# Kernel optimization log

Measured on AMD Instinct MI355X. Metric: run time of the kernel, lower is better.

Reference implementation:

```python
import jax, jax.numpy as jnp
import numpy as np

EMBED_DIM = 512
SMOOTH = 4.0        # args.lambda_softmax
LAMBDA_LSE = 6.0    # args.lambda_lse
LEAKY_SLOPE = 0.1
EPS = 1e-8


def setup_inputs() -> dict:
    key = jax.random.key(0)
    k1, k2, k3 = jax.random.split(key, 3)
    n_contract, n_region = 32, 256
    n_law, max_len = 32, 256
    contracts = jax.random.normal(k1, (n_contract, n_region, EMBED_DIM), jnp.float32)
    laws = jax.random.normal(k2, (n_law, max_len, EMBED_DIM), jnp.float32)
    law_lens = jax.random.randint(k3, (n_law,), 128, max_len + 1, jnp.int32)
    return {"contracts": contracts, "laws": laws, "law_lens": law_lens}


def reference(contracts, laws, law_lens):
    # contracts: [C, R, D], laws: [N, L, D], law_lens: [N]
    n_law, max_len, d = laws.shape
    # mask[n, l] = 1 if word l is within law n's true length
    mask = (jnp.arange(max_len)[None, :] < law_lens[:, None]).astype(contracts.dtype)

    # attn = law @ contract^T / sqrt(D): [N, C, L, R]
    attn = jnp.einsum('nld,crd->nclr', laws, contracts) / jnp.sqrt(jnp.float32(d))
    attn = jax.nn.leaky_relu(attn, LEAKY_SLOPE)
    # l2norm over region dim (per law-word row)
    attn = attn / (jnp.linalg.norm(attn, axis=-1, keepdims=True) + EPS)
    attn = jax.nn.softmax(attn, axis=-1) * SMOOTH
    # zero out contributions from padded law words (ragged lengths)
    attn = attn * mask[:, None, :, None]

    # weighted_law: [N, C, R, D]
    wlaw = jnp.einsum('nld,nclr->ncrd', laws, attn)

    # cosine similarity along D: [N, C, R]
    w12 = jnp.sum(contracts[None] * wlaw, axis=-1)
    w1 = jnp.linalg.norm(contracts, axis=-1)[None]          # [1, C, R]
    w2 = jnp.linalg.norm(wlaw, axis=-1)                      # [N, C, R]
    sim = w12 / jnp.maximum(w1 * w2, EPS)

    # LogSumExp aggregation over regions -> [N, C]
    row_sim = jnp.log(jnp.sum(jnp.exp(sim * LAMBDA_LSE), axis=-1)) / LAMBDA_LSE
    # concatenate per-law columns -> [C, N]
    return row_sim.T
```

## Files before the change

### kernel.cpp

```cpp
#include <hip/hip_runtime.h>
#include <hip/hip_bf16.h>

#define CN 32
#define RN 256
#define DN 512
#define NN 32
#define LN 256

#define STAGE_OFF 131072
#define SMEM_TOTAL 163840

typedef short v8s __attribute__((ext_vector_type(8)));
typedef float v4f __attribute__((ext_vector_type(4)));
typedef const __attribute__((address_space(1))) void* gas1_t;
typedef __attribute__((address_space(3))) void* las3_t;

__device__ __forceinline__ void gl2lds16(const void* g, void* l) {
  __builtin_amdgcn_global_load_lds((gas1_t)g, (las3_t)l, 16, 0, 0);
}

__device__ __forceinline__ unsigned short f2bf(float x) {
  unsigned int u = __float_as_uint(x);
  u = (u + 0x7fffu + ((u >> 16) & 1u)) >> 16;
  return (unsigned short)u;
}
__device__ __forceinline__ float bf2f(unsigned short h) {
  return __uint_as_float(((unsigned int)h) << 16);
}

__device__ __forceinline__ unsigned int pkbf(float a, float b) {
  __hip_bfloat162 h = __float22bfloat162_rn(make_float2(a, b));
  unsigned int u;
  __builtin_memcpy(&u, &h, sizeof(u));
  return u;
}

__device__ __forceinline__ const v8s* stgFrag(const unsigned short* buf, int r,
                                              int quad) {
  return (const v8s*)(buf + r * 32 + ((quad ^ ((r >> 1) & 3)) << 3));
}

__device__ __forceinline__ int satIdx(int r, int col) {
  return (r << 8) | ((((col >> 3) ^ (r & 7)) << 3) | (col & 7));
}

__device__ __forceinline__ v8s ldFrag64(const float* buf, int r, int cp) {
  const float* p = buf + r * 64 + (((cp + r) & 7) << 3);
  const float4 x0 = ((const float4*)p)[0];
  const float4 x1 = ((const float4*)p)[1];
  unsigned short h[8];
  h[0] = f2bf(x0.x); h[1] = f2bf(x0.y); h[2] = f2bf(x0.z); h[3] = f2bf(x0.w);
  h[4] = f2bf(x1.x); h[5] = f2bf(x1.y); h[6] = f2bf(x1.z); h[7] = f2bf(x1.w);
  return *(v8s*)h;
}

__global__ __launch_bounds__(512) void setup_kernel(
    const float* __restrict__ con, const float* __restrict__ laws,
    unsigned short* __restrict__ lawsB, unsigned short* __restrict__ conB,
    float* __restrict__ cnorm, unsigned short* __restrict__ G) {
  const int bid = blockIdx.x;
  const int t = threadIdx.x;
  if (bid < 256) {
    __shared__ float slice[256 * 64];
    const int n = bid >> 3;
    const int m0 = (bid & 7) << 5;
    const int lane = t & 63;
    const int w = t >> 6;
    const int quad = lane >> 4;
    const int l16 = lane & 15;
    const int rg = w >> 2;
    const int cg = w & 3;
    const float* lawN = laws + n * (LN * DN);

    v4f acc[4];
#pragma unroll
    for (int b = 0; b < 4; ++b) acc[b] = (v4f){0.f, 0.f, 0.f, 0.f};

    for (int ch = 0; ch < 8; ++ch) {
      const int dk = ch << 6;
      __syncthreads();
#pragma unroll
      for (int i = 0; i < 8; ++i) {
        const int s = i * 512 + t;
        const int row = s >> 4;
        const int p = s & 15;
        const int srcCol = ((((p >> 1) - row) & 7) << 3) + ((p & 1) << 2);
        gl2lds16(lawN + row * DN + dk + srcCol, (char*)slice + s * 16);
      }
      __syncthreads();
#pragma unroll
      for (int step = 0; step < 2; ++step) {
        const int cp = quad + (step << 2);
        v8s af = ldFrag64(slice, m0 + rg * 16 + l16, cp);
#pragma unroll
        for (int ct = 0; ct < 4; ++ct) {
          v8s bf = ldFrag64(slice, cg * 64 + ct * 16 + l16, cp);
          acc[ct] = __builtin_amdgcn_mfma_f32_16x16x32_bf16(af, bf, acc[ct], 0, 0, 0);
        }
      }
    }
    unsigned short* g = G + n * (LN * LN);
#pragma unroll
    for (int ct = 0; ct < 4; ++ct)
#pragma unroll
      for (int reg = 0; reg < 4; ++reg) {
        const int l = m0 + rg * 16 + quad * 4 + reg;
        g[l * LN + cg * 64 + ct * 16 + l16] = f2bf(acc[ct][reg]);
      }
  } else if (bid < 1280) {
    const int r = (bid - 256) * 8 + (t >> 6);
    const int lane = t & 63;
    const float4* src = (const float4*)(con + r * DN + lane * 8);
    float4 x0 = src[0], x1 = src[1];
    unsigned short h[8];
    h[0] = f2bf(x0.x); h[1] = f2bf(x0.y); h[2] = f2bf(x0.z); h[3] = f2bf(x0.w);
    h[4] = f2bf(x1.x); h[5] = f2bf(x1.y); h[6] = f2bf(x1.z); h[7] = f2bf(x1.w);
    *(v8s*)(conB + r * DN + lane * 8) = *(v8s*)h;
    float s = x0.x * x0.x + x0.y * x0.y + x0.z * x0.z + x0.w * x0.w +
              x1.x * x1.x + x1.y * x1.y + x1.z * x1.z + x1.w * x1.w;
#pragma unroll
    for (int m = 1; m < 64; m <<= 1) s += __shfl_xor(s, m, 64);
    if (lane == 0) cnorm[r] = sqrtf(s);
  } else {
    const int off = (bid - 1280) * 4096 + t * 8;
    const float4* src = (const float4*)(laws + off);
    float4 x0 = src[0], x1 = src[1];
    unsigned short h[8];
    h[0] = f2bf(x0.x); h[1] = f2bf(x0.y); h[2] = f2bf(x0.z); h[3] = f2bf(x0.w);
    h[4] = f2bf(x1.x); h[5] = f2bf(x1.y); h[6] = f2bf(x1.z); h[7] = f2bf(x1.w);
    *(v8s*)(lawsB + off) = *(v8s*)h;
  }
}

__global__ __launch_bounds__(512, 2) void main_kernel(
    const int* __restrict__ law_lens, const unsigned short* __restrict__ lawsB,
    const unsigned short* __restrict__ conB, const unsigned short* __restrict__ Gm,
    const float* __restrict__ cnorm, float* __restrict__ out) {
  extern __shared__ char smem[];
  unsigned short* sAt = (unsigned short*)smem;
  char* stage = smem + STAGE_OFF;

  const int bid = blockIdx.x;
  const int n = bid >> 5;
  const int c = bid & 31;
  const int t = threadIdx.x;
  const int lane = t & 63;
  const int w = t >> 6;
  const int quad = lane >> 4;
  const int l16 = lane & 15;
  const int sub = t & 3;
  const int rQ = t >> 2;
  const int subx = sub ^ ((rQ >> 1) & 3);
  const int len = law_lens[n];
  const int nCh = (len + 31) >> 5;
  const bool active = (w * 32) < len;

  const unsigned short* lawN = lawsB + n * (LN * DN);
  const unsigned short* conC = conB + c * (RN * DN);
  const unsigned short* Gn = Gm + n * (LN * LN);

  float w12p[16];
#pragma unroll
  for (int i = 0; i < 16; ++i) w12p[i] = 0.f;

  {
    const unsigned short* a0p = lawN + (w * 32 + l16) * DN + quad * 8;
    const unsigned short* a1p = a0p + 16 * DN;

    v4f acc[2][16];
#pragma unroll
    for (int a = 0; a < 2; ++a)
#pragma unroll
      for (int b = 0; b < 16; ++b) acc[a][b] = (v4f){0.f, 0.f, 0.f, 0.f};

#pragma unroll
    for (int i = 0; i < 2; ++i)
      gl2lds16(conC + (i * 128 + rQ) * DN + subx * 8,
               stage + i * 8192 + t * 16);

    for (int ch = 0; ch < 16; ++ch) {
      const int dk = ch << 5;
      __syncthreads();
      v8s af0 = *(const v8s*)(a0p + dk);
      v8s af1 = *(const v8s*)(a1p + dk);
      __builtin_amdgcn_sched_barrier(0);
      if (ch < 15) {
        char* dst = stage + ((ch + 1) & 1) * 16384;
#pragma unroll
        for (int i = 0; i < 2; ++i)
          gl2lds16(conC + (i * 128 + rQ) * DN + (dk + 32) + subx * 8,
                   dst + i * 8192 + t * 16);
      }
      __builtin_amdgcn_sched_barrier(0);
      if (active) {
        const unsigned short* cs =
            (const unsigned short*)(stage + (ch & 1) * 16384);
#pragma unroll
        for (int rt = 0; rt < 16; ++rt) {
          v8s bf = *stgFrag(cs, rt * 16 + l16, quad);
          acc[0][rt] = __builtin_amdgcn_mfma_f32_16x16x32_bf16(af0, bf, acc[0][rt], 0, 0, 0);
          acc[1][rt] = __builtin_amdgcn_mfma_f32_16x16x32_bf16(af1, bf, acc[1][rt], 0, 0, 0);
        }
      }
    }

    __syncthreads();

#pragma unroll
    for (int i = 0; i < 2; ++i)
      gl2lds16(Gn + (i * 128 + rQ) * LN + subx * 8, stage + i * 8192 + t * 16);

    if (active) {
#pragma unroll
      for (int tl = 0; tl < 2; ++tl) {
        unsigned int pk[16][2];
        float a0s[16];
#pragma unroll
        for (int reg = 0; reg < 4; ++reg) {
          const int lg = w * 32 + tl * 16 + quad * 4 + reg;
          float ss = 0.f;
#pragma unroll
          for (int rt = 0; rt < 16; ++rt) {
            const float v = acc[tl][rt][reg] * 0.04419417382415922f;
            const float lv = v > 0.f ? v : 0.1f * v;
            ss += lv * lv;
          }
#pragma unroll
          for (int m = 1; m < 16; m <<= 1) ss += __shfl_xor(ss, m, 64);
          const float inv = 1.f / (sqrtf(ss) + 1e-8f);
          float e[16];
          float den = 0.f;
#pragma unroll
          for (int rt = 0; rt < 16; ++rt) {
            const float v = acc[tl][rt][reg] * 0.04419417382415922f;
            const float lv = v > 0.f ? v : 0.1f * v;
            e[rt] = __expf(lv * inv);
            den += e[rt];
          }
#pragma unroll
          for (int m = 1; m < 16; m <<= 1) den += __shfl_xor(den, m, 64);
          const float sc = (lg < len) ? 4.f / den : 0.f;
#pragma unroll
          for (int rt = 0; rt < 16; ++rt) {
            const float v = acc[tl][rt][reg] * 0.04419417382415922f;
            const float a = e[rt] * sc;
            w12p[rt] += a * v;
            if (reg & 1)
              pk[rt][reg >> 1] = pkbf(a0s[rt], a);
            else
              a0s[rt] = a;
          }
        }
        const int lg0 = w * 32 + tl * 16 + quad * 4;
#pragma unroll
        for (int rt = 0; rt < 16; ++rt)
          *(uint2*)(sAt + satIdx(rt * 16 + l16, lg0)) = *(uint2*)pk[rt];
      }
    } else {
      uint2 z;
      z.x = 0u;
      z.y = 0u;
#pragma unroll
      for (int tl = 0; tl < 2; ++tl) {
        const int lg0 = w * 32 + tl * 16 + quad * 4;
#pragma unroll
        for (int rt = 0; rt < 16; ++rt)
          *(uint2*)(sAt + satIdx(rt * 16 + l16, lg0)) = z;
      }
    }
  }

#pragma unroll
  for (int rt = 0; rt < 16; ++rt) {
    w12p[rt] += __shfl_xor(w12p[rt], 16, 64);
    w12p[rt] += __shfl_xor(w12p[rt], 32, 64);
  }

  float nsv[2][4];
  {
    v4f acc[2][16];
#pragma unroll
    for (int a = 0; a < 2; ++a)
#pragma unroll
      for (int b = 0; b < 16; ++b) acc[a][b] = (v4f){0.f, 0.f, 0.f, 0.f};

    for (int ch = 0; ch < nCh; ++ch) {
      const int lk = ch << 5;
      __syncthreads();
      v8s af0 = *(const v8s*)(sAt + satIdx(w * 32 + l16, lk + quad * 8));
      v8s af1 = *(const v8s*)(sAt + satIdx(w * 32 + 16 + l16, lk + quad * 8));
      __builtin_amdgcn_sched_barrier(0);
      if (ch < nCh - 1) {
        char* dst = stage + ((ch + 1) & 1) * 16384;
#pragma unroll
        for (int i = 0; i < 2; ++i)
          gl2lds16(Gn + (i * 128 + rQ) * LN + (lk + 32) + subx * 8,
                   dst + i * 8192 + t * 16);
      }
      __builtin_amdgcn_sched_barrier(0);
      const unsigned short* gs =
          (const unsigned short*)(stage + (ch & 1) * 16384);
#pragma unroll
      for (int lt = 0; lt < 16; ++lt) {
        v8s bf = *stgFrag(gs, lt * 16 + l16, quad);
        acc[0][lt] = __builtin_amdgcn_mfma_f32_16x16x32_bf16(af0, bf, acc[0][lt], 0, 0, 0);
        acc[1][lt] = __builtin_amdgcn_mfma_f32_16x16x32_bf16(af1, bf, acc[1][lt], 0, 0, 0);
      }
    }
#pragma unroll
    for (int tl = 0; tl < 2; ++tl) {
#pragma unroll
      for (int reg = 0; reg < 4; ++reg) {
        const int r = w * 32 + tl * 16 + quad * 4 + reg;
        float s = 0.f;
#pragma unroll
        for (int lt = 0; lt < 16; ++lt)
          s += acc[tl][lt][reg] * bf2f(sAt[satIdx(r, lt * 16 + l16)]);
#pragma unroll
        for (int m = 1; m < 16; m <<= 1) s += __shfl_xor(s, m, 64);
        nsv[tl][reg] = s;
      }
    }
  }

  float* w12s = (float*)stage;
  float* nsqS = (float*)(stage + 8192);
  float* red = (float*)(stage + 9216);
  __syncthreads();
  if (l16 == 0) {
#pragma unroll
    for (int tl = 0; tl < 2; ++tl)
#pragma unroll
      for (int reg = 0; reg < 4; ++reg)
        nsqS[w * 32 + tl * 16 + quad * 4 + reg] = nsv[tl][reg];
  }
  if (lane < 16) {
#pragma unroll
    for (int rt = 0; rt < 16; ++rt) w12s[w * 256 + rt * 16 + lane] = w12p[rt];
  }
  __syncthreads();
  float p = 0.f;
  if (t < 256) {
    float w12 = 0.f;
#pragma unroll
    for (int i = 0; i < 8; ++i) w12 += w12s[i * 256 + t];
    const float w1 = cnorm[c * RN + t];
    const float w2 = sqrtf(fmaxf(nsqS[t], 0.f));
    const float sim = (w12 * 22.627416997969522f) / fmaxf(w1 * w2, 1e-8f);
    p = __expf(6.f * sim);
  }
#pragma unroll
  for (int m = 1; m < 64; m <<= 1) p += __shfl_xor(p, m, 64);
  if (lane == 0) red[w] = p;
  __syncthreads();
  if (t == 0) {
    float s = 0.f;
#pragma unroll
    for (int i = 0; i < 8; ++i) s += red[i];
    out[c * NN + n] = logf(s) / 6.f;
  }
}

extern "C" void kernel_launch(void* const* d_in, const int* in_sizes, int n_in,
                              void* d_out, int out_size, void* d_ws, size_t ws_size,
                              hipStream_t stream) {
  (void)in_sizes; (void)n_in; (void)out_size;
  const float* contracts = (const float*)d_in[0];
  const float* laws = (const float*)d_in[1];
  const int* law_lens = (const int*)d_in[2];
  float* out = (float*)d_out;

  unsigned short* lawsB = (unsigned short*)d_ws;
  unsigned short* conB = lawsB + NN * LN * DN;
  unsigned short* G = conB + CN * RN * DN;
  float* cnorm = (float*)(G + NN * LN * LN);
  if (ws_size < (size_t)21004288) return;

  hipFuncSetAttribute((const void*)main_kernel,
                      hipFuncAttributeMaxDynamicSharedMemorySize, SMEM_TOTAL);

  setup_kernel<<<2304, 512, 0, stream>>>(contracts, laws, lawsB, conB, cnorm,
                                         G);
  main_kernel<<<1024, 512, SMEM_TOTAL, stream>>>(law_lens, lawsB, conB, G,
                                                 cnorm, out);
}
```

Baseline: 244.9 us.

## Switch Gram-matrix norm pass to FP8 MFMA with scaled fp8 storage

Stores the law Gram matrix G and the per-row attention matrix in FP8 (with 0.5 and 64 scale factors) instead of bf16. The second GEMM, which computes the squared norm of the weighted law via attn·G·attnᵀ, now uses fp8 MFMA. This halves the LDS footprint (98 KB instead of 160 KB), the G staging traffic and the global G buffer. It also skips law-fragment loads for inactive waves. The cost is reduced precision in the norm computation, which may affect accuracy.

```diff
diff --git a/kernel.cpp b/kernel.cpp
--- a/kernel.cpp
+++ b/kernel.cpp
@@ -7,8 +7,8 @@
 #define NN 32
 #define LN 256
 
-#define STAGE_OFF 131072
-#define SMEM_TOTAL 163840
+#define STAGE_OFF 65536
+#define SMEM_TOTAL 98304
 
 typedef short v8s __attribute__((ext_vector_type(8)));
 typedef float v4f __attribute__((ext_vector_type(4)));
@@ -24,23 +24,13 @@
   u = (u + 0x7fffu + ((u >> 16) & 1u)) >> 16;
   return (unsigned short)u;
 }
-__device__ __forceinline__ float bf2f(unsigned short h) {
-  return __uint_as_float(((unsigned int)h) << 16);
-}
-
-__device__ __forceinline__ unsigned int pkbf(float a, float b) {
-  __hip_bfloat162 h = __float22bfloat162_rn(make_float2(a, b));
-  unsigned int u;
-  __builtin_memcpy(&u, &h, sizeof(u));
-  return u;
-}
 
 __device__ __forceinline__ const v8s* stgFrag(const unsigned short* buf, int r,
                                               int quad) {
   return (const v8s*)(buf + r * 32 + ((quad ^ ((r >> 1) & 3)) << 3));
 }
 
-__device__ __forceinline__ int satIdx(int r, int col) {
+__device__ __forceinline__ int sat8Idx(int r, int col) {
   return (r << 8) | ((((col >> 3) ^ (r & 7)) << 3) | (col & 7));
 }
 
@@ -57,7 +47,7 @@
 __global__ __launch_bounds__(512) void setup_kernel(
     const float* __restrict__ con, const float* __restrict__ laws,
     unsigned short* __restrict__ lawsB, unsigned short* __restrict__ conB,
-    float* __restrict__ cnorm, unsigned short* __restrict__ G) {
+    float* __restrict__ cnorm, unsigned char* __restrict__ G8) {
   const int bid = blockIdx.x;
   const int t = threadIdx.x;
   if (bid < 256) {
@@ -99,13 +89,15 @@
         }
       }
     }
-    unsigned short* g = G + n * (LN * LN);
+    unsigned char* g = G8 + n * (LN * LN);
 #pragma unroll
     for (int ct = 0; ct < 4; ++ct)
 #pragma unroll
       for (int reg = 0; reg < 4; ++reg) {
         const int l = m0 + rg * 16 + quad * 4 + reg;
-        g[l * LN + cg * 64 + ct * 16 + l16] = f2bf(acc[ct][reg]);
+        const float v = acc[ct][reg] * 0.5f;
+        const int p = __builtin_amdgcn_cvt_pk_fp8_f32(v, v, 0, false);
+        g[l * LN + cg * 64 + ct * 16 + l16] = (unsigned char)(p & 0xff);
       }
   } else if (bid < 1280) {
     const int r = (bid - 256) * 8 + (t >> 6);
@@ -134,10 +126,10 @@
 
 __global__ __launch_bounds__(512, 2) void main_kernel(
     const int* __restrict__ law_lens, const unsigned short* __restrict__ lawsB,
-    const unsigned short* __restrict__ conB, const unsigned short* __restrict__ Gm,
+    const unsigned short* __restrict__ conB, const unsigned char* __restrict__ G8m,
     const float* __restrict__ cnorm, float* __restrict__ out) {
   extern __shared__ char smem[];
-  unsigned short* sAt = (unsigned short*)smem;
+  unsigned char* sAt8 = (unsigned char*)smem;
   char* stage = smem + STAGE_OFF;
 
   const int bid = blockIdx.x;
@@ -157,7 +149,10 @@
 
   const unsigned short* lawN = lawsB + n * (LN * DN);
   const unsigned short* conC = conB + c * (RN * DN);
-  const unsigned short* Gn = Gm + n * (LN * LN);
+  const unsigned char* G8n = G8m + n * (LN * LN);
+
+  const int g8row = t >> 1;
+  const int g8half = (t & 1) ^ ((g8row >> 2) & 1);
 
   float w12p[16];
 #pragma unroll
@@ -181,8 +176,11 @@
     for (int ch = 0; ch < 16; ++ch) {
       const int dk = ch << 5;
       __syncthreads();
-      v8s af0 = *(const v8s*)(a0p + dk);
-      v8s af1 = *(const v8s*)(a1p + dk);
+      v8s af0, af1;
+      if (active) {
+        af0 = *(const v8s*)(a0p + dk);
+        af1 = *(const v8s*)(a1p + dk);
+      }
       __builtin_amdgcn_sched_barrier(0);
       if (ch < 15) {
         char* dst = stage + ((ch + 1) & 1) * 16384;
@@ -206,14 +204,12 @@
 
     __syncthreads();
 
-#pragma unroll
-    for (int i = 0; i < 2; ++i)
-      gl2lds16(Gn + (i * 128 + rQ) * LN + subx * 8, stage + i * 8192 + t * 16);
+    gl2lds16(G8n + g8row * LN + g8half * 16, stage + t * 16);
 
     if (active) {
 #pragma unroll
       for (int tl = 0; tl < 2; ++tl) {
-        unsigned int pk[16][2];
+        unsigned int pk[16];
         float a0s[16];
 #pragma unroll
         for (int reg = 0; reg < 4; ++reg) {
@@ -245,27 +241,31 @@
             const float v = acc[tl][rt][reg] * 0.04419417382415922f;
             const float a = e[rt] * sc;
             w12p[rt] += a * v;
-            if (reg & 1)
-              pk[rt][reg >> 1] = pkbf(a0s[rt], a);
+            const float ax = a * 64.f;
+            if (reg == 0)
+              a0s[rt] = ax;
+            else if (reg == 1)
+              pk[rt] = (unsigned int)__builtin_amdgcn_cvt_pk_fp8_f32(
+                  a0s[rt], ax, 0, false);
+            else if (reg == 2)
+              a0s[rt] = ax;
             else
-              a0s[rt] = a;
+              pk[rt] = (unsigned int)__builtin_amdgcn_cvt_pk_fp8_f32(
+                  a0s[rt], ax, (int)pk[rt], true);
           }
         }
         const int lg0 = w * 32 + tl * 16 + quad * 4;
 #pragma unroll
         for (int rt = 0; rt < 16; ++rt)
-          *(uint2*)(sAt + satIdx(rt * 16 + l16, lg0)) = *(uint2*)pk[rt];
+          *(unsigned int*)(sAt8 + sat8Idx(rt * 16 + l16, lg0)) = pk[rt];
       }
     } else {
-      uint2 z;
-      z.x = 0u;
-      z.y = 0u;
 #pragma unroll
       for (int tl = 0; tl < 2; ++tl) {
         const int lg0 = w * 32 + tl * 16 + quad * 4;
 #pragma unroll
         for (int rt = 0; rt < 16; ++rt)
-          *(uint2*)(sAt + satIdx(rt * 16 + l16, lg0)) = z;
+          *(unsigned int*)(sAt8 + sat8Idx(rt * 16 + l16, lg0)) = 0u;
       }
     }
   }
@@ -287,24 +287,21 @@
     for (int ch = 0; ch < nCh; ++ch) {
       const int lk = ch << 5;
       __syncthreads();
-      v8s af0 = *(const v8s*)(sAt + satIdx(w * 32 + l16, lk + quad * 8));
-      v8s af1 = *(const v8s*)(sAt + satIdx(w * 32 + 16 + l16, lk + quad * 8));
+      long af0 = *(const long*)(sAt8 + sat8Idx(w * 32 + l16, lk + quad * 8));
+      long af1 = *(const long*)(sAt8 + sat8Idx(w * 32 + 16 + l16, lk + quad * 8));
       __builtin_amdgcn_sched_barrier(0);
-      if (ch < nCh - 1) {
-        char* dst = stage + ((ch + 1) & 1) * 16384;
-#pragma unroll
-        for (int i = 0; i < 2; ++i)
-          gl2lds16(Gn + (i * 128 + rQ) * LN + (lk + 32) + subx * 8,
-                   dst + i * 8192 + t * 16);
-      }
+      if (ch < nCh - 1)
+        gl2lds16(G8n + g8row * LN + (lk + 32) + g8half * 16,
+                 stage + ((ch + 1) & 1) * 8192 + t * 16);
       __builtin_amdgcn_sched_barrier(0);
-      const unsigned short* gs =
-          (const unsigned short*)(stage + (ch & 1) * 16384);
+      const unsigned char* gs = (const unsigned char*)(stage + (ch & 1) * 8192);
 #pragma unroll
       for (int lt = 0; lt < 16; ++lt) {
-        v8s bf = *stgFrag(gs, lt * 16 + l16, quad);
-        acc[0][lt] = __builtin_amdgcn_mfma_f32_16x16x32_bf16(af0, bf, acc[0][lt], 0, 0, 0);
-        acc[1][lt] = __builtin_amdgcn_mfma_f32_16x16x32_bf16(af1, bf, acc[1][lt], 0, 0, 0);
+        const int rr = lt * 16 + l16;
+        long bf = *(const long*)(gs + rr * 32 +
+                                 ((quad ^ (((rr >> 2) & 1) << 1)) << 3));
+        acc[0][lt] = __builtin_amdgcn_mfma_f32_16x16x32_fp8_fp8(af0, bf, acc[0][lt], 0, 0, 0);
+        acc[1][lt] = __builtin_amdgcn_mfma_f32_16x16x32_fp8_fp8(af1, bf, acc[1][lt], 0, 0, 0);
       }
     }
 #pragma unroll
@@ -314,18 +311,20 @@
         const int r = w * 32 + tl * 16 + quad * 4 + reg;
         float s = 0.f;
 #pragma unroll
-        for (int lt = 0; lt < 16; ++lt)
-          s += acc[tl][lt][reg] * bf2f(sAt[satIdx(r, lt * 16 + l16)]);
+        for (int lt = 0; lt < 16; ++lt) {
+          const int b = sAt8[sat8Idx(r, lt * 16 + l16)];
+          s += acc[tl][lt][reg] * __builtin_amdgcn_cvt_f32_fp8(b, 0);
+        }
 #pragma unroll
         for (int m = 1; m < 16; m <<= 1) s += __shfl_xor(s, m, 64);
-        nsv[tl][reg] = s;
-      }
-    }
-  }
-
-  float* w12s = (float*)stage;
-  float* nsqS = (float*)(stage + 8192);
-  float* red = (float*)(stage + 9216);
+        nsv[tl][reg] = s * (1.f / 2048.f);
+      }
+    }
+  }
+
+  float* w12s = (float*)(stage + 16384);
+  float* nsqS = (float*)(stage + 24576);
+  float* red = (float*)(stage + 25600);
   __syncthreads();
   if (l16 == 0) {
 #pragma unroll
@@ -372,15 +371,15 @@
 
   unsigned short* lawsB = (unsigned short*)d_ws;
   unsigned short* conB = lawsB + NN * LN * DN;
-  unsigned short* G = conB + CN * RN * DN;
-  float* cnorm = (float*)(G + NN * LN * LN);
-  if (ws_size < (size_t)21004288) return;
+  unsigned char* G8 = (unsigned char*)(conB + CN * RN * DN);
+  float* cnorm = (float*)(G8 + NN * LN * LN);
+  if (ws_size < (size_t)18907136) return;
 
   hipFuncSetAttribute((const void*)main_kernel,
                       hipFuncAttributeMaxDynamicSharedMemorySize, SMEM_TOTAL);
 
   setup_kernel<<<2304, 512, 0, stream>>>(contracts, laws, lawsB, conB, cnorm,
-                                         G);
-  main_kernel<<<1024, 512, SMEM_TOTAL, stream>>>(law_lens, lawsB, conB, G,
+                                         G8);
+  main_kernel<<<1024, 512, SMEM_TOTAL, stream>>>(law_lens, lawsB, conB, G8,
                                                  cnorm, out);
 }
```

New measurement: 253.0 us. 3.3% more time.
